# Kernel optimization log

Measured on AMD Instinct MI355X. Metric: run time of the kernel, lower is better.

Reference implementation:

```python
import jax, jax.numpy as jnp
import numpy as np

B, T, DIM, HEADS = 4, 2048, 1024, 16
D_K = DIM // HEADS


def setup_inputs() -> dict:
    key = jax.random.key(0)
    ks = jax.random.split(key, 5)
    x = jax.random.normal(ks[0], (B, T, DIM), dtype=jnp.float32)
    # nn.Linear params: weight [out, in], bias [out]
    w_qkv = jax.random.normal(ks[1], (3 * DIM, DIM), dtype=jnp.float32) / np.sqrt(DIM)
    b_qkv = jax.random.normal(ks[2], (3 * DIM,), dtype=jnp.float32) * 0.02
    w_out = jax.random.normal(ks[3], (DIM, DIM), dtype=jnp.float32) / np.sqrt(DIM)
    b_out = jax.random.normal(ks[4], (DIM,), dtype=jnp.float32) * 0.02
    # causal mask, broadcast over batch and heads: [1, 1, T, T]
    mask = jnp.tril(jnp.ones((T, T), dtype=jnp.int32))[None, None]
    return {"x": x, "w_qkv": w_qkv, "b_qkv": b_qkv, "w_out": w_out, "b_out": b_out, "mask": mask}


def reference(x, w_qkv, b_qkv, w_out, b_out, mask):
    Bb, Tt, D = x.shape
    # fused QKV projection: [B,T,3D] -> [3,B,H,T,d_k]
    qkv = (x @ w_qkv.T + b_qkv).reshape(Bb, Tt, 3, HEADS, D_K).transpose(2, 0, 3, 1, 4)
    q, k, v = qkv[0], qkv[1], qkv[2]
    scores = jnp.einsum("bhqd,bhkd->bhqk", q, k) / jnp.sqrt(jnp.float32(D_K))
    scores = jnp.where(mask == 0, -jnp.inf, scores)
    attn = jax.nn.softmax(scores, axis=-1)  # [B,H,T,T]
    context = jnp.einsum("bhqk,bhkd->bhqd", attn, v)
    context = context.transpose(0, 2, 1, 3).reshape(Bb, Tt, D)
    return context @ w_out.T + b_out
```

## Files before the change

kernel.cpp:

```cpp
#include <hip/hip_runtime.h>

typedef unsigned short ushort_t;
typedef __bf16 bf16x8 __attribute__((ext_vector_type(8)));
typedef float f32x4 __attribute__((ext_vector_type(4)));

#define BB 4
#define TT 2048
#define DIMD 1024
#define NH 16
#define DK 64
#define MROWS (BB * TT)
#define NQKV (3 * DIMD)

__device__ __forceinline__ ushort_t f2b(float f) {
  __bf16 h = (__bf16)f;
  union { __bf16 h; ushort_t u; } c; c.h = h; return c.u;
}
__device__ __forceinline__ float fexp2(float x) {
  float r;
  asm("v_exp_f32 %0, %1" : "=v"(r) : "v"(x));
  return r;
}

__device__ __forceinline__ void gload_lds16(const void* g, void* l) {
  __builtin_amdgcn_global_load_lds(
      (const __attribute__((address_space(1))) void*)g,
      (__attribute__((address_space(3))) void*)l,
      16, 0, 0);
}

__global__ __launch_bounds__(256) void cast_f32_bf16(
    const float* __restrict__ in, ushort_t* __restrict__ out, int n)
{
  const int i = (blockIdx.x * 256 + threadIdx.x) * 8;
  if (i >= n) return;
  float4 a = *(const float4*)(in + i);
  float4 b = *(const float4*)(in + i + 4);
  ushort_t o[8];
  o[0] = f2b(a.x); o[1] = f2b(a.y); o[2] = f2b(a.z); o[3] = f2b(a.w);
  o[4] = f2b(b.x); o[5] = f2b(b.y); o[6] = f2b(b.z); o[7] = f2b(b.w);
  *(uint4*)(out + i) = *(const uint4*)o;
}

template <bool OUT_F32>
__global__ __launch_bounds__(256) void gemm_bt_bias(
    const ushort_t* __restrict__ A, const ushort_t* __restrict__ W,
    const float* __restrict__ bias, void* __restrict__ Cp,
    int M, int N, int K)
{
  __shared__ __align__(16) ushort_t As[128 * 32];
  __shared__ __align__(16) ushort_t Bs[128 * 32];

  const int tid = threadIdx.x;
  const int wave = tid >> 6, lane = tid & 63;
  const int tiles_n = N >> 7;
  const int bm = blockIdx.x / tiles_n, bn = blockIdx.x % tiles_n;
  const int row0 = bm << 7, col0 = bn << 7;
  const int wm = (wave >> 1) << 6;
  const int wn = (wave & 1) << 6;
  const int fr = lane & 15;
  const int fk = (lane >> 4) << 3;
  const int g4 = (lane >> 4) << 2;

  const int sr = lane >> 2;
  const int csw = fk ^ (((fr >> 1) & 3) << 3);

  f32x4 acc[4][4] = {};

  for (int k0 = 0; k0 < K; k0 += 32) {
    __syncthreads();
#pragma unroll
    for (int p = 0; p < 2; ++p) {
      const int e = (wave << 9) + (p << 11);
      const int r = (e >> 5) + sr;
      const int c = ((lane & 3) << 3) ^ (((r >> 1) & 3) << 3);
      gload_lds16(A + (size_t)(row0 + r) * K + (k0 + c), As + e);
      gload_lds16(W + (size_t)(col0 + r) * K + (k0 + c), Bs + e);
    }
    __syncthreads();

    bf16x8 af[4], bw[4];
#pragma unroll
    for (int i = 0; i < 4; ++i) {
      af[i] = *(const bf16x8*)&As[(wm + (i << 4) + fr) * 32 + csw];
      bw[i] = *(const bf16x8*)&Bs[(wn + (i << 4) + fr) * 32 + csw];
    }
#pragma unroll
    for (int mi = 0; mi < 4; ++mi)
#pragma unroll
      for (int ni = 0; ni < 4; ++ni)
        acc[mi][ni] = __builtin_amdgcn_mfma_f32_16x16x32_bf16(af[mi], bw[ni], acc[mi][ni], 0, 0, 0);
  }

#pragma unroll
  for (int ni = 0; ni < 4; ++ni) {
    const int col = col0 + wn + (ni << 4) + fr;
    const float bv = bias[col];
#pragma unroll
    for (int mi = 0; mi < 4; ++mi)
#pragma unroll
      for (int r = 0; r < 4; ++r) {
        const size_t row = (size_t)(row0 + wm + (mi << 4) + g4 + r);
        if constexpr (OUT_F32)
          ((float*)Cp)[row * (size_t)N + col] = acc[mi][ni][r] + bv;
        else
          ((ushort_t*)Cp)[row * (size_t)N + col] = f2b(acc[mi][ni][r] + bv);
      }
  }
}

#define C1 0.18033688011112042f
__global__ __launch_bounds__(512, 4) void attn_fused(
    const ushort_t* __restrict__ qkv, ushort_t* __restrict__ ctx)
{
  __shared__ __align__(16) ushort_t Qs[128 * 64];
  __shared__ __align__(16) ushort_t Ks[2][64 * 64];
  __shared__ __align__(16) ushort_t Vt[64 * 64];
  __shared__ __align__(16) ushort_t Ps[8][16 * 64];

  const int tid = threadIdx.x, wave = tid >> 6, lane = tid & 63;
  const int fr = lane & 15;
  const int g  = lane >> 4;
  const int fk = g << 3;
  const int g4 = g << 2;

  const int bid = blockIdx.x;
  const int bq  = (bid >> 3) & 7;
  const int G   = (bid & 7) | ((bid >> 6) << 3);
  const int h   = G & 15;
  const int b   = G >> 4;

  const int srl = lane >> 3;
  const int scc = ((lane & 7) ^ srl) << 3;
  const int vr  = tid >> 3;
  const int vc  = (tid & 7) << 3;
  const int rsw = (fr & 7) << 3;

  const ushort_t* Kg = qkv + (size_t)b * TT * NQKV + DIMD + h * DK;
  const ushort_t* Vg = qkv + (size_t)b * TT * NQKV + 2 * DIMD + h * DK;

#pragma unroll 1
  for (int t = 0; t < 2; ++t) {
    const int qt = t ? (15 - bq) : bq;
    const int ktmax = 2 * qt + 1;
    const int diag  = 2 * qt + (wave >> 2);
    const size_t qrow0 = (size_t)b * TT + (size_t)qt * 128;

    __syncthreads();

    const ushort_t* Qg = qkv + qrow0 * NQKV + h * DK;
#pragma unroll
    for (int pp = 0; pp < 2; ++pp) {
      const int e  = (wave << 9) + (pp << 12);
      const int rr = (e >> 6) + srl;
      gload_lds16(Qg + (size_t)rr * NQKV + scc, Qs + e);
    }
    {
      const int e  = wave << 9;
      const int rr = (wave << 3) + srl;
      gload_lds16(Kg + (size_t)rr * NQKV + scc, Ks[0] + e);
    }
    uint4 va = *(const uint4*)(Vg + (size_t)vr * NQKV + vc);
    asm volatile("s_waitcnt vmcnt(0)" ::: "memory");
    __syncthreads();

    bf16x8 aqr[2];
#pragma unroll
    for (int ks = 0; ks < 2; ++ks)
      aqr[ks] = *(const bf16x8*)&Qs[((wave << 4) + fr) * 64 + (((ks << 5) + fk) ^ rsw)];

    const int qrow = (qt << 7) + (wave << 4) + fr;
    float mrow = -1e30f, lrow = 0.f;
    f32x4 oacc[4] = {};
    int cur = 0;

    for (int kt = 0; kt <= ktmax; ++kt) {
      {
        __align__(16) ushort_t tmp[8];
        *(uint4*)tmp = va;
#pragma unroll
        for (int j = 0; j < 8; ++j) {
          const int d  = vc + j;
          const int hh = (d & 7) ^ ((d >> 3) & 7);
          Vt[d * 64 + (vr ^ (hh << 3))] = tmp[j];
        }
      }
      if (kt < ktmax) {
        const size_t krow = (size_t)(kt + 1) << 6;
        const int e  = wave << 9;
        const int rr = (wave << 3) + srl;
        gload_lds16(Kg + (krow + rr) * NQKV + scc, Ks[cur ^ 1] + e);
        va = *(const uint4*)(Vg + (krow + vr) * NQKV + vc);
      }
      asm volatile("s_waitcnt lgkmcnt(0)" ::: "memory");
      __builtin_amdgcn_s_barrier();

      if (kt <= diag) {
        f32x4 s[4] = {};
        __builtin_amdgcn_s_setprio(1);
#pragma unroll
        for (int ks = 0; ks < 2; ++ks)
#pragma unroll
          for (int ni = 0; ni < 4; ++ni) {
            const bf16x8 bk = *(const bf16x8*)&Ks[cur][((ni << 4) + fr) * 64 + (((ks << 5) + fk) ^ rsw)];
            s[ni] = __builtin_amdgcn_mfma_f32_16x16x32_bf16(bk, aqr[ks], s[ni], 0, 0, 0);
          }
        __builtin_amdgcn_s_setprio(0);

        if (kt == diag) {
          const int kb = kt << 6;
#pragma unroll
          for (int ni = 0; ni < 4; ++ni)
#pragma unroll
            for (int r = 0; r < 4; ++r) {
              const int kc = kb + (ni << 4) + g4 + r;
              if (kc > qrow) s[ni][r] = -1e30f;
            }
        }

        float rm = -1e30f;
#pragma unroll
        for (int ni = 0; ni < 4; ++ni) {
          const float m01 = fmaxf(s[ni][0], s[ni][1]);
          const float m23 = fmaxf(s[ni][2], s[ni][3]);
          rm = fmaxf(rm, fmaxf(m01, m23));
        }
        rm = fmaxf(rm, __shfl_xor(rm, 16, 64));
        rm = fmaxf(rm, __shfl_xor(rm, 32, 64));

        if (__any(rm > mrow + 64.f)) {
          const float mn = fmaxf(mrow, rm);
          const float corr = fexp2((mrow - mn) * C1);
          mrow = mn;
          lrow *= corr;
#pragma unroll
          for (int ni = 0; ni < 4; ++ni) oacc[ni] *= corr;
        }
        const float nm2 = -mrow * C1;
        float rs = 0.f;
#pragma unroll
        for (int ni = 0; ni < 4; ++ni)
#pragma unroll
          for (int r = 0; r < 4; ++r) {
            const float pe = fexp2(fmaf(s[ni][r], C1, nm2));
            s[ni][r] = pe;
            rs += pe;
          }
        rs += __shfl_xor(rs, 16, 64);
        rs += __shfl_xor(rs, 32, 64);
        lrow += rs;

#pragma unroll
        for (int ni = 0; ni < 4; ++ni) {
          ushort_t o4[4];
#pragma unroll
          for (int r = 0; r < 4; ++r) o4[r] = f2b(s[ni][r]);
          *(uint2*)&Ps[wave][fr * 64 + (((ni << 4) + g4) ^ rsw)] = *(const uint2*)o4;
        }
        asm volatile("s_waitcnt lgkmcnt(0)" ::: "memory");
        __builtin_amdgcn_sched_barrier(0);

        __builtin_amdgcn_s_setprio(1);
#pragma unroll
        for (int ks = 0; ks < 2; ++ks) {
          const bf16x8 ap = *(const bf16x8*)&Ps[wave][fr * 64 + (((ks << 5) + fk) ^ rsw)];
#pragma unroll
          for (int ni = 0; ni < 4; ++ni) {
            const int hh = (fr & 7) ^ ((2 * ni + (fr >> 3)) & 7);
            const bf16x8 bv = *(const bf16x8*)&Vt[((ni << 4) + fr) * 64 + (((ks << 5) + fk) ^ (hh << 3))];
            oacc[ni] = __builtin_amdgcn_mfma_f32_16x16x32_bf16(bv, ap, oacc[ni], 0, 0, 0);
          }
        }
        __builtin_amdgcn_s_setprio(0);
      }

      if (kt < ktmax) {
        asm volatile("s_waitcnt vmcnt(0)" ::: "memory");
        __syncthreads();
      }
      cur ^= 1;
    }

    const float inv = 1.f / lrow;
    ushort_t* crow = ctx + (qrow0 + (wave << 4) + fr) * DIMD + h * DK;
#pragma unroll
    for (int ni = 0; ni < 4; ++ni) {
      ushort_t o4[4];
#pragma unroll
      for (int r = 0; r < 4; ++r) o4[r] = f2b(oacc[ni][r] * inv);
      *(uint2*)&crow[(ni << 4) + g4] = *(const uint2*)o4;
    }
  }
}

extern "C" void kernel_launch(void* const* d_in, const int* in_sizes, int n_in,
                              void* d_out, int out_size, void* d_ws, size_t ws_size,
                              hipStream_t stream) {
  const float* x     = (const float*)d_in[0];
  const float* w_qkv = (const float*)d_in[1];
  const float* b_qkv = (const float*)d_in[2];
  const float* w_out = (const float*)d_in[3];
  const float* b_out = (const float*)d_in[4];

  const size_t need = 36u * 1024 * 1024 * sizeof(ushort_t);
  if (ws_size < need) return;

  ushort_t* qkv = (ushort_t*)d_ws;
  ushort_t* xb  = qkv + (size_t)MROWS * NQKV;
  ushort_t* wqb = xb  + (size_t)MROWS * DIMD;
  ushort_t* wob = wqb + (size_t)NQKV * DIMD;
  ushort_t* ctx = xb;
  float*    out = (float*)d_out;

  cast_f32_bf16<<<dim3(MROWS * DIMD / 2048), dim3(256), 0, stream>>>(x, xb, MROWS * DIMD);
  cast_f32_bf16<<<dim3(NQKV * DIMD / 2048), dim3(256), 0, stream>>>(w_qkv, wqb, NQKV * DIMD);
  cast_f32_bf16<<<dim3(DIMD * DIMD / 2048), dim3(256), 0, stream>>>(w_out, wob, DIMD * DIMD);
  gemm_bt_bias<false><<<dim3((MROWS / 128) * (NQKV / 128)), dim3(256), 0, stream>>>(
      xb, wqb, b_qkv, (void*)qkv, MROWS, NQKV, DIMD);
  attn_fused<<<dim3(BB * NH * 8), dim3(512), 0, stream>>>(qkv, ctx);
  gemm_bt_bias<true><<<dim3((MROWS / 128) * (DIMD / 128)), dim3(256), 0, stream>>>(
      ctx, wob, b_out, (void*)out, MROWS, DIMD, DIMD);
}
```

Measured before the change: 184.5 us.

## Add 256x256-tile double-buffered GEMM for the QKV projection

Adds a new bf16 GEMM kernel that uses 256x256 output tiles with 512 threads and a K-step of 64. It double-buffers the A and W tiles in LDS through direct global-to-LDS loads, with an XOR swizzle against bank conflicts. It also remaps block IDs across the 8 XCDs and raises wave priority around the MFMA loop. The QKV projection now uses this kernel, which should raise data reuse and overlap loads with compute. The cost is 128KB of LDS per block, so one block per CU, and a grid of 384 blocks that leaves a partial wave tail.

```diff
diff --git a/kernel.cpp b/kernel.cpp
--- a/kernel.cpp
+++ b/kernel.cpp
@@ -43,6 +43,107 @@
 }
 
 template <bool OUT_F32>
+__global__ __launch_bounds__(512, 2) void gemm_bt_bias_256(
+    const ushort_t* __restrict__ A, const ushort_t* __restrict__ W,
+    const float* __restrict__ bias, void* __restrict__ Cp,
+    int M, int N, int K)
+{
+  __shared__ __align__(16) ushort_t As[2][256 * 64];
+  __shared__ __align__(16) ushort_t Bs[2][256 * 64];
+
+  const int tid = threadIdx.x;
+  const int wave = tid >> 6, lane = tid & 63;
+  const int tiles_n = N >> 8;
+  const int nwg = (M >> 8) * tiles_n;
+  int bid = blockIdx.x;
+  { const int q = nwg >> 3; bid = (bid & 7) * q + (bid >> 3); }
+  const int bm = bid / tiles_n, bn = bid % tiles_n;
+  const int row0 = bm << 8, col0 = bn << 8;
+  const int wm = (wave >> 2) << 7;
+  const int wn = (wave & 3) << 6;
+  const int fr = lane & 15;
+  const int g  = lane >> 4;
+  const int g4 = g << 2;
+  const int fk = g << 3;
+  const int rsw = (fr & 7) << 3;
+
+  const int str = tid >> 3;
+  const int stc = ((tid & 7) ^ (str & 7)) << 3;
+
+  const ushort_t* Ab = A + (size_t)row0 * K;
+  const ushort_t* Wb = W + (size_t)col0 * K;
+
+#define STAGE256(t)                                                           \
+  {                                                                           \
+    const int _buf = (t) & 1;                                                 \
+    const size_t _k0 = (size_t)(t) << 6;                                      \
+    _Pragma("unroll")                                                         \
+    for (int p = 0; p < 4; ++p) {                                             \
+      const int e = (p << 12) + (wave << 9);                                  \
+      const int r = (p << 6) + str;                                           \
+      gload_lds16(Ab + (size_t)r * K + _k0 + stc, &As[_buf][e]);              \
+      gload_lds16(Wb + (size_t)r * K + _k0 + stc, &Bs[_buf][e]);              \
+    }                                                                         \
+  }
+
+  const int NT = K >> 6;
+  STAGE256(0);
+  STAGE256(1);
+
+  f32x4 acc[8][4] = {};
+
+  for (int t = 0; t < NT; ++t) {
+    if (t < NT - 1) asm volatile("s_waitcnt vmcnt(8)" ::: "memory");
+    else            asm volatile("s_waitcnt vmcnt(0)" ::: "memory");
+    __builtin_amdgcn_s_barrier();
+
+    const int buf = t & 1;
+    bf16x8 af[8][2], bw[4][2];
+#pragma unroll
+    for (int i = 0; i < 8; ++i)
+#pragma unroll
+      for (int s = 0; s < 2; ++s)
+        af[i][s] = *(const bf16x8*)&As[buf][(wm + (i << 4) + fr) * 64 + (((s << 5) + fk) ^ rsw)];
+#pragma unroll
+    for (int j = 0; j < 4; ++j)
+#pragma unroll
+      for (int s = 0; s < 2; ++s)
+        bw[j][s] = *(const bf16x8*)&Bs[buf][(wn + (j << 4) + fr) * 64 + (((s << 5) + fk) ^ rsw)];
+    asm volatile("s_waitcnt lgkmcnt(0)" ::: "memory");
+    __builtin_amdgcn_s_barrier();
+
+    if (t + 2 < NT) STAGE256(t + 2);
+
+    __builtin_amdgcn_s_setprio(1);
+#pragma unroll
+    for (int s = 0; s < 2; ++s)
+#pragma unroll
+      for (int i = 0; i < 8; ++i)
+#pragma unroll
+        for (int j = 0; j < 4; ++j)
+          acc[i][j] = __builtin_amdgcn_mfma_f32_16x16x32_bf16(af[i][s], bw[j][s], acc[i][j], 0, 0, 0);
+    __builtin_amdgcn_s_setprio(0);
+  }
+#undef STAGE256
+
+#pragma unroll
+  for (int j = 0; j < 4; ++j) {
+    const int col = col0 + wn + (j << 4) + fr;
+    const float bv = bias[col];
+#pragma unroll
+    for (int i = 0; i < 8; ++i)
+#pragma unroll
+      for (int r = 0; r < 4; ++r) {
+        const size_t row = (size_t)(row0 + wm + (i << 4) + g4 + r);
+        if constexpr (OUT_F32)
+          ((float*)Cp)[row * (size_t)N + col] = acc[i][j][r] + bv;
+        else
+          ((ushort_t*)Cp)[row * (size_t)N + col] = f2b(acc[i][j][r] + bv);
+      }
+  }
+}
+
+template <bool OUT_F32>
 __global__ __launch_bounds__(256) void gemm_bt_bias(
     const ushort_t* __restrict__ A, const ushort_t* __restrict__ W,
     const float* __restrict__ bias, void* __restrict__ Cp,
@@ -315,7 +416,7 @@
   cast_f32_bf16<<<dim3(MROWS * DIMD / 2048), dim3(256), 0, stream>>>(x, xb, MROWS * DIMD);
   cast_f32_bf16<<<dim3(NQKV * DIMD / 2048), dim3(256), 0, stream>>>(w_qkv, wqb, NQKV * DIMD);
   cast_f32_bf16<<<dim3(DIMD * DIMD / 2048), dim3(256), 0, stream>>>(w_out, wob, DIMD * DIMD);
-  gemm_bt_bias<false><<<dim3((MROWS / 128) * (NQKV / 128)), dim3(256), 0, stream>>>(
+  gemm_bt_bias_256<false><<<dim3((MROWS / 256) * (NQKV / 256)), dim3(512), 0, stream>>>(
       xb, wqb, b_qkv, (void*)qkv, MROWS, NQKV, DIMD);
   attn_fused<<<dim3(BB * NH * 8), dim3(512), 0, stream>>>(qkv, ctx);
   gemm_bt_bias<true><<<dim3((MROWS / 128) * (DIMD / 128)), dim3(256), 0, stream>>>(
```

New measurement: 183.1 us. Within noise of the previous version (-0.7%).

## Pipeline GEMMs with triple-buffered LDS and 128x256 tiles

Applied to the files above, without the earlier changes.

Replaces the projection GEMM with a 512-thread kernel using 128x256 tiles and a three-stage LDS ring. Global-to-LDS loads for tile t+2 are issued while tile t is being multiplied, and synchronisation uses vmcnt waits plus a raw barrier instead of two __syncthreads per iteration. Block IDs are remapped to group neighbouring tiles for better L2 reuse, and MFMA sections run at raised wave priority. The cost is more LDS per block, which may limit occupancy, and grid-size assumptions: the nwg/8 remap is only a valid permutation when the tile count is divisible by 8.

```diff
diff --git a/kernel.cpp b/kernel.cpp
--- a/kernel.cpp
+++ b/kernel.cpp
@@ -43,68 +43,112 @@
 }
 
 template <bool OUT_F32>
-__global__ __launch_bounds__(256) void gemm_bt_bias(
+__global__ __launch_bounds__(512, 4) void gemm_bt_pipe(
     const ushort_t* __restrict__ A, const ushort_t* __restrict__ W,
     const float* __restrict__ bias, void* __restrict__ Cp,
     int M, int N, int K)
 {
-  __shared__ __align__(16) ushort_t As[128 * 32];
-  __shared__ __align__(16) ushort_t Bs[128 * 32];
+  __shared__ __align__(16) ushort_t As[3][128 * 32];
+  __shared__ __align__(16) ushort_t Bs[3][256 * 32];
 
   const int tid = threadIdx.x;
   const int wave = tid >> 6, lane = tid & 63;
-  const int tiles_n = N >> 7;
-  const int bm = blockIdx.x / tiles_n, bn = blockIdx.x % tiles_n;
-  const int row0 = bm << 7, col0 = bn << 7;
-  const int wm = (wave >> 1) << 6;
-  const int wn = (wave & 1) << 6;
+  const int tiles_n = N >> 8;
+  const int nwg = (M >> 7) * tiles_n;
+  int bid = blockIdx.x;
+  { const int q = nwg >> 3; bid = (bid & 7) * q + (bid >> 3); }
+  const int bm = bid / tiles_n, bn = bid % tiles_n;
+  const int row0 = bm << 7, col0 = bn << 8;
+  const int wm = (wave >> 2) << 6;
+  const int wn = (wave & 3) << 6;
   const int fr = lane & 15;
-  const int fk = (lane >> 4) << 3;
-  const int g4 = (lane >> 4) << 2;
-
-  const int sr = lane >> 2;
-  const int csw = fk ^ (((fr >> 1) & 3) << 3);
+  const int g  = lane >> 4;
+  const int g4 = g << 2;
+  const int csw = (g ^ (fr >> 2)) << 3;
+
+  const int srow = lane >> 2;
+  const int scol = ((lane & 3) ^ ((lane >> 4) & 3)) << 3;
+  const int lbase = wave << 9;
+
+  const ushort_t* Ag  = A + (size_t)(row0 + (wave << 4) + srow) * K + scol;
+  const ushort_t* Wg0 = W + (size_t)(col0 + (wave << 4) + srow) * K + scol;
+  const ushort_t* Wg1 = Wg0 + (size_t)128 * K;
+
+#define STAGE_P(kt, buf)                                                      \
+  {                                                                           \
+    const size_t _k = (size_t)(kt) << 5;                                      \
+    gload_lds16(Ag + _k,  &As[buf][lbase]);                                   \
+    gload_lds16(Wg0 + _k, &Bs[buf][lbase]);                                   \
+    gload_lds16(Wg1 + _k, &Bs[buf][4096 + lbase]);                            \
+  }
+
+  const int NT = K >> 5;
+  STAGE_P(0, 0);
+  STAGE_P(1, 1);
 
   f32x4 acc[4][4] = {};
-
-  for (int k0 = 0; k0 < K; k0 += 32) {
-    __syncthreads();
-#pragma unroll
-    for (int p = 0; p < 2; ++p) {
-      const int e = (wave << 9) + (p << 11);
-      const int r = (e >> 5) + sr;
-      const int c = ((lane & 3) << 3) ^ (((r >> 1) & 3) << 3);
-      gload_lds16(A + (size_t)(row0 + r) * K + (k0 + c), As + e);
-      gload_lds16(W + (size_t)(col0 + r) * K + (k0 + c), Bs + e);
-    }
-    __syncthreads();
-
-    bf16x8 af[4], bw[4];
-#pragma unroll
-    for (int i = 0; i < 4; ++i) {
-      af[i] = *(const bf16x8*)&As[(wm + (i << 4) + fr) * 32 + csw];
-      bw[i] = *(const bf16x8*)&Bs[(wn + (i << 4) + fr) * 32 + csw];
-    }
-#pragma unroll
-    for (int mi = 0; mi < 4; ++mi)
-#pragma unroll
-      for (int ni = 0; ni < 4; ++ni)
-        acc[mi][ni] = __builtin_amdgcn_mfma_f32_16x16x32_bf16(af[mi], bw[ni], acc[mi][ni], 0, 0, 0);
+  int cr = 0, st = 2;
+
+  for (int t = 0; t < NT; ++t) {
+    if (t + 1 < NT) asm volatile("s_waitcnt vmcnt(3)" ::: "memory");
+    else            asm volatile("s_waitcnt vmcnt(0)" ::: "memory");
+    __builtin_amdgcn_s_barrier();
+
+    const ushort_t* as_ = As[cr];
+    const ushort_t* bs_ = Bs[cr];
+    bf16x8 af0 = *(const bf16x8*)&as_[(wm +      fr) * 32 + csw];
+    bf16x8 af1 = *(const bf16x8*)&as_[(wm + 16 + fr) * 32 + csw];
+    bf16x8 bw0 = *(const bf16x8*)&bs_[(wn +      fr) * 32 + csw];
+    bf16x8 bw1 = *(const bf16x8*)&bs_[(wn + 16 + fr) * 32 + csw];
+    bf16x8 bw2 = *(const bf16x8*)&bs_[(wn + 32 + fr) * 32 + csw];
+    bf16x8 bw3 = *(const bf16x8*)&bs_[(wn + 48 + fr) * 32 + csw];
+    if (t + 2 < NT) STAGE_P(t + 2, st);
+    asm volatile("s_waitcnt lgkmcnt(0)" ::: "memory");
+    __builtin_amdgcn_sched_barrier(0);
+    __builtin_amdgcn_s_setprio(1);
+    acc[0][0] = __builtin_amdgcn_mfma_f32_16x16x32_bf16(af0, bw0, acc[0][0], 0, 0, 0);
+    acc[0][1] = __builtin_amdgcn_mfma_f32_16x16x32_bf16(af0, bw1, acc[0][1], 0, 0, 0);
+    acc[0][2] = __builtin_amdgcn_mfma_f32_16x16x32_bf16(af0, bw2, acc[0][2], 0, 0, 0);
+    acc[0][3] = __builtin_amdgcn_mfma_f32_16x16x32_bf16(af0, bw3, acc[0][3], 0, 0, 0);
+    acc[1][0] = __builtin_amdgcn_mfma_f32_16x16x32_bf16(af1, bw0, acc[1][0], 0, 0, 0);
+    acc[1][1] = __builtin_amdgcn_mfma_f32_16x16x32_bf16(af1, bw1, acc[1][1], 0, 0, 0);
+    acc[1][2] = __builtin_amdgcn_mfma_f32_16x16x32_bf16(af1, bw2, acc[1][2], 0, 0, 0);
+    acc[1][3] = __builtin_amdgcn_mfma_f32_16x16x32_bf16(af1, bw3, acc[1][3], 0, 0, 0);
+    __builtin_amdgcn_s_setprio(0);
+
+    bf16x8 af2 = *(const bf16x8*)&as_[(wm + 32 + fr) * 32 + csw];
+    bf16x8 af3 = *(const bf16x8*)&as_[(wm + 48 + fr) * 32 + csw];
+    asm volatile("s_waitcnt lgkmcnt(0)" ::: "memory");
+    __builtin_amdgcn_sched_barrier(0);
+    __builtin_amdgcn_s_setprio(1);
+    acc[2][0] = __builtin_amdgcn_mfma_f32_16x16x32_bf16(af2, bw0, acc[2][0], 0, 0, 0);
+    acc[2][1] = __builtin_amdgcn_mfma_f32_16x16x32_bf16(af2, bw1, acc[2][1], 0, 0, 0);
+    acc[2][2] = __builtin_amdgcn_mfma_f32_16x16x32_bf16(af2, bw2, acc[2][2], 0, 0, 0);
+    acc[2][3] = __builtin_amdgcn_mfma_f32_16x16x32_bf16(af2, bw3, acc[2][3], 0, 0, 0);
+    acc[3][0] = __builtin_amdgcn_mfma_f32_16x16x32_bf16(af3, bw0, acc[3][0], 0, 0, 0);
+    acc[3][1] = __builtin_amdgcn_mfma_f32_16x16x32_bf16(af3, bw1, acc[3][1], 0, 0, 0);
+    acc[3][2] = __builtin_amdgcn_mfma_f32_16x16x32_bf16(af3, bw2, acc[3][2], 0, 0, 0);
+    acc[3][3] = __builtin_amdgcn_mfma_f32_16x16x32_bf16(af3, bw3, acc[3][3], 0, 0, 0);
+    __builtin_amdgcn_s_setprio(0);
+
+    ++cr; if (cr == 3) cr = 0;
+    ++st; if (st == 3) st = 0;
   }
-
-#pragma unroll
-  for (int ni = 0; ni < 4; ++ni) {
-    const int col = col0 + wn + (ni << 4) + fr;
+#undef STAGE_P
+
+#pragma unroll
+  for (int j = 0; j < 4; ++j) {
+    const int col = col0 + wn + (j << 4) + fr;
     const float bv = bias[col];
 #pragma unroll
-    for (int mi = 0; mi < 4; ++mi)
+    for (int i = 0; i < 4; ++i)
 #pragma unroll
       for (int r = 0; r < 4; ++r) {
-        const size_t row = (size_t)(row0 + wm + (mi << 4) + g4 + r);
+        const size_t row = (size_t)(row0 + wm + (i << 4) + g4 + r);
         if constexpr (OUT_F32)
-          ((float*)Cp)[row * (size_t)N + col] = acc[mi][ni][r] + bv;
+          ((float*)Cp)[row * (size_t)N + col] = acc[i][j][r] + bv;
         else
-          ((ushort_t*)Cp)[row * (size_t)N + col] = f2b(acc[mi][ni][r] + bv);
+          ((ushort_t*)Cp)[row * (size_t)N + col] = f2b(acc[i][j][r] + bv);
       }
   }
 }
@@ -315,9 +359,9 @@
   cast_f32_bf16<<<dim3(MROWS * DIMD / 2048), dim3(256), 0, stream>>>(x, xb, MROWS * DIMD);
   cast_f32_bf16<<<dim3(NQKV * DIMD / 2048), dim3(256), 0, stream>>>(w_qkv, wqb, NQKV * DIMD);
   cast_f32_bf16<<<dim3(DIMD * DIMD / 2048), dim3(256), 0, stream>>>(w_out, wob, DIMD * DIMD);
-  gemm_bt_bias<false><<<dim3((MROWS / 128) * (NQKV / 128)), dim3(256), 0, stream>>>(
+  gemm_bt_pipe<false><<<dim3((MROWS / 128) * (NQKV / 256)), dim3(512), 0, stream>>>(
       xb, wqb, b_qkv, (void*)qkv, MROWS, NQKV, DIMD);
   attn_fused<<<dim3(BB * NH * 8), dim3(512), 0, stream>>>(qkv, ctx);
-  gemm_bt_bias<true><<<dim3((MROWS / 128) * (DIMD / 128)), dim3(256), 0, stream>>>(
+  gemm_bt_pipe<true><<<dim3((MROWS / 128) * (DIMD / 256)), dim3(512), 0, stream>>>(
       ctx, wob, b_out, (void*)out, MROWS, DIMD, DIMD);
 }
```

Measured after the change: 176.8 us. -4.2%, faster.
